# Performance work log

Measured on AMD Instinct MI355X. Metric: run time of the kernel, lower is better.

The kernel has to match this reference:

```python
import jax, jax.numpy as jnp
import numpy as np

D_MODEL = 2048
N_HEADS = 16
HEAD_DIM = D_MODEL // N_HEADS
SCALE = HEAD_DIM ** -0.5


def setup_inputs() -> dict:
    key = jax.random.key(0)
    ks = jax.random.split(key, 9)
    B, L, D = 4, 4096, D_MODEL
    s = 1.0 / np.sqrt(D)
    inp = {"x": jax.random.normal(ks[0], (B, L, D), dtype=jnp.float32)}
    inp["Wq"] = jax.random.normal(ks[1], (D, D), dtype=jnp.float32) * s
    inp["bq"] = jnp.zeros((D,), dtype=jnp.float32)
    inp["Wk"] = jax.random.normal(ks[2], (D, D), dtype=jnp.float32) * s
    inp["bk"] = jnp.zeros((D,), dtype=jnp.float32)
    inp["Wv"] = jax.random.normal(ks[3], (D, D), dtype=jnp.float32) * s
    inp["bv"] = jnp.zeros((D,), dtype=jnp.float32)
    inp["Wo"] = jax.random.normal(ks[4], (D, D), dtype=jnp.float32) * s
    inp["bo"] = jnp.zeros((D,), dtype=jnp.float32)
    return inp


def reference(x, Wq, bq, Wk, bk, Wv, bv, Wo, bo):
    B, L, D = x.shape
    H, Hd = N_HEADS, HEAD_DIM
    # projections (torch Linear: x @ W.T + b)
    q = jnp.einsum('bld,ed->ble', x, Wq) + bq
    k = jnp.einsum('bld,ed->ble', x, Wk) + bk
    v = jnp.einsum('bld,ed->ble', x, Wv) + bv
    phi_q = jax.nn.elu(q) + 1.0
    phi_k = jax.nn.elu(k) + 1.0
    # (B, L, H, Hd)
    phi_q = phi_q.reshape(B, L, H, Hd)
    phi_k = phi_k.reshape(B, L, H, Hd)
    v = v.reshape(B, L, H, Hd)
    # elementwise prefix sum over sequence dim
    kv_sum = jnp.cumsum(phi_k * v, axis=1)  # (B, L, H, Hd)
    context = (phi_q * kv_sum).reshape(B, L, D) * SCALE
    return jnp.einsum('bld,ed->ble', context, Wo) + bo
```

## Files before the change

### kernel.cpp

```cpp
#include <hip/hip_runtime.h>
#include <hip/hip_bf16.h>
#include <cstdint>
#include <cstddef>

typedef __bf16 bf16x8 __attribute__((ext_vector_type(8)));
typedef __bf16 bf16x4 __attribute__((ext_vector_type(4)));
typedef float  f32x4  __attribute__((ext_vector_type(4)));

#define D_MODEL 2048
#define SEQ     4096
#define BATCH   4
#define M_TOK   (BATCH * SEQ)
#define ATTN_SCALE 0.08838834764831845f

#define BM 256
#define BN 256
#define BK 64
#define NT (D_MODEL / BK)
#define BUF_BYTES 65536
#define B_OFF     32768

#define NSEG   64
#define SEGLEN (SEQ / NSEG)

__device__ __forceinline__ void async_load16(const void* g, void* l) {
    __builtin_amdgcn_global_load_lds(
        (const __attribute__((address_space(1))) unsigned int*)g,
        (__attribute__((address_space(3))) unsigned int*)l,
        16, 0, 0);
}

__device__ __forceinline__ void wg_barrier() {
    __builtin_amdgcn_sched_barrier(0);
    __builtin_amdgcn_s_barrier();
    __builtin_amdgcn_sched_barrier(0);
}

#define VMCNT(n) asm volatile("s_waitcnt vmcnt(" #n ")" ::: "memory")

__global__ __launch_bounds__(256) void k_cast_bf16(const float* __restrict__ in,
                                                   __bf16* __restrict__ out,
                                                   int n8) {
    int i = blockIdx.x * 256 + threadIdx.x;
    if (i >= n8) return;
    const float4* in4 = (const float4*)in;
    float4 a = in4[2 * i];
    float4 b = in4[2 * i + 1];
    bf16x8 o;
    o[0] = (__bf16)a.x; o[1] = (__bf16)a.y; o[2] = (__bf16)a.z; o[3] = (__bf16)a.w;
    o[4] = (__bf16)b.x; o[5] = (__bf16)b.y; o[6] = (__bf16)b.z; o[7] = (__bf16)b.w;
    ((bf16x8*)out)[i] = o;
}

__global__ __launch_bounds__(256) void k_cast_w4(const float* __restrict__ w0,
                                                 const float* __restrict__ w1,
                                                 const float* __restrict__ w2,
                                                 const float* __restrict__ w3,
                                                 __bf16* __restrict__ out, int n8) {
    const float* srcs[4] = {w0, w1, w2, w3};
    const float* in = srcs[blockIdx.y];
    __bf16* o = out + (size_t)blockIdx.y * (size_t)n8 * 8;
    int i = blockIdx.x * 256 + threadIdx.x;
    if (i >= n8) return;
    const float4* in4 = (const float4*)in;
    float4 a = in4[2 * i];
    float4 b = in4[2 * i + 1];
    bf16x8 v;
    v[0] = (__bf16)a.x; v[1] = (__bf16)a.y; v[2] = (__bf16)a.z; v[3] = (__bf16)a.w;
    v[4] = (__bf16)b.x; v[5] = (__bf16)b.y; v[6] = (__bf16)b.z; v[7] = (__bf16)b.w;
    ((bf16x8*)o)[i] = v;
}

template <int PHI, typename OUT_T>
__device__ __forceinline__ void gemm256(const __bf16* __restrict__ A,
                                        const __bf16* __restrict__ Bm,
                                        const float* __restrict__ bias,
                                        OUT_T* __restrict__ C,
                                        int bx, int by) {
    extern __shared__ bf16x8 lds_dyn[];
    char* lds = (char*)lds_dyn;

    const int tid  = threadIdx.x;
    const int lane = tid & 63;
    const int wave = tid >> 6;
    const int wr = wave & 1;
    const int wc = wave >> 1;
    const long bm = (long)by * BM;
    const long bn = (long)bx * BN;
    const int  K = D_MODEL, N = D_MODEL;

    const int sp  = tid & 7;
    const int rA0 = tid >> 3;
    const int rA1 = 64 + rA0;
    const int rBe = ((tid >> 8) << 6) + ((tid >> 3) & 31);
    const int rBo = rBe + 32;
    const __bf16* gA0 = A  + (bm + rA0) * (long)K + ((sp ^ (rA0 & 7)) << 3);
    const __bf16* gA1 = A  + (bm + rA1) * (long)K + ((sp ^ (rA1 & 7)) << 3);
    const __bf16* gBe = Bm + (bn + rBe) * (long)K + ((sp ^ (rBe & 7)) << 3);
    const __bf16* gBo = Bm + (bn + rBo) * (long)K + ((sp ^ (rBo & 7)) << 3);
    const long l128K = 128L * K;
    const int lA0 = tid * 16;
    const int lA1 = 8192 + tid * 16;
    const int lBe = B_OFF + ((tid >> 8) << 13) + (((tid >> 3) & 31) << 7) + sp * 16;
    const int lBo = lBe + 4096;

    auto issue2 = [&](const __bf16* g, int ldsByte) {
        async_load16(g, lds + ldsByte);
        async_load16(g + l128K, lds + ldsByte + 16384);
    };

    issue2(gA0, lA0);              gA0 += BK;
    issue2(gBe, lBe);              gBe += BK;
    issue2(gBo, lBo);              gBo += BK;
    issue2(gA1, lA1);              gA1 += BK;
    issue2(gA0, lA0 + BUF_BYTES);  gA0 += BK;
    issue2(gBe, lBe + BUF_BYTES);  gBe += BK;
    VMCNT(8);
    wg_barrier();

    const int lm   = lane & 15;
    const int ksel = lane >> 4;
    const int m3   = lm & 7;
    const int clo  = ksel ^ (m3 & 3);
    const int cb0  = ((((m3 >> 2) << 2) | clo) << 4);
    const int cb1  = ((((1 ^ (m3 >> 2)) << 2) | clo) << 4);
    const int aBase = (wr * 128 + lm) * 128;
    const int bBase = B_OFF + (wc * 64 + lm) * 128;

    f32x4 acc[8][4] = {};

    int cur = 0;
#pragma unroll 1
    for (int t = 0; t < NT; ++t) {
#pragma unroll
        for (int p = 0; p < 4; ++p) {
            const int qm = p >> 1, qn = p & 1;
            bf16x8 af[4][2], bfr[2][2];
#pragma unroll
            for (int i = 0; i < 4; ++i) {
                const char* rp = lds + cur + aBase + (qm * 64 + i * 16) * 128;
                af[i][0] = *(const bf16x8*)(rp + cb0);
                af[i][1] = *(const bf16x8*)(rp + cb1);
            }
#pragma unroll
            for (int j = 0; j < 2; ++j) {
                const char* rp = lds + cur + bBase + (qn * 32 + j * 16) * 128;
                bfr[j][0] = *(const bf16x8*)(rp + cb0);
                bfr[j][1] = *(const bf16x8*)(rp + cb1);
            }
            if (p == 0 && t + 1 < NT) { issue2(gBo, lBo + (cur ^ BUF_BYTES)); gBo += BK; }
            if (p == 1 && t + 1 < NT) { issue2(gA1, lA1 + (cur ^ BUF_BYTES)); gA1 += BK; }
            if (p == 2 && t + 2 < NT) { issue2(gA0, lA0 + cur); gA0 += BK; }
            if (p == 3 && t + 2 < NT) { issue2(gBe, lBe + cur); gBe += BK; }
            wg_barrier();
            __builtin_amdgcn_s_setprio(1);
#pragma unroll
            for (int s = 0; s < 2; ++s)
#pragma unroll
                for (int i = 0; i < 4; ++i)
#pragma unroll
                    for (int j = 0; j < 2; ++j)
                        acc[qm * 4 + i][qn * 2 + j] = __builtin_amdgcn_mfma_f32_16x16x32_bf16(
                            af[i][s], bfr[j][s], acc[qm * 4 + i][qn * 2 + j], 0, 0, 0);
            __builtin_amdgcn_s_setprio(0);
            if (p == 0 || p == 1) { if (t < NT - 1) VMCNT(8); }
            if (p == 3) { if (t < NT - 2) VMCNT(8); else if (t == NT - 2) VMCNT(0); }
            wg_barrier();
        }
        cur ^= BUF_BYTES;
    }

    const int r0m = (lane >> 4) << 2;
#pragma unroll
    for (int i = 0; i < 8; ++i) {
        const long mg = bm + wr * 128 + i * 16 + r0m;
#pragma unroll
        for (int j = 0; j < 4; ++j) {
            const long ng = bn + wc * 64 + j * 16 + lm;
            const float bia = bias[ng];
#pragma unroll
            for (int r = 0; r < 4; ++r) {
                float v = acc[i][j][r] + bia;
                if (PHI) v = (v > 0.f) ? (v + 1.f) : __expf(v);
                C[(mg + r) * (long)N + ng] = (OUT_T)v;
            }
        }
    }
}

__global__ __launch_bounds__(512, 2) void k_gemm_qkv(
    const __bf16* __restrict__ xb,
    const __bf16* __restrict__ wq, const __bf16* __restrict__ wk, const __bf16* __restrict__ wv,
    const float* __restrict__ bq, const float* __restrict__ bk, const float* __restrict__ bv,
    __bf16* __restrict__ oq, __bf16* __restrict__ ok, __bf16* __restrict__ ov) {
    const int flat = blockIdx.y * 8 + blockIdx.x;
    const int swz  = (flat & 7) * 64 + (flat >> 3);
    const int bx = swz & 7, by = swz >> 3;
    const int z = blockIdx.z;
    const __bf16* W = (z == 0) ? wq : (z == 1) ? wk : wv;
    const float*  b = (z == 0) ? bq : (z == 1) ? bk : bv;
    __bf16*       o = (z == 0) ? oq : (z == 1) ? ok : ov;
    if (z < 2)
        gemm256<1, __bf16>(xb, W, b, o, bx, by);
    else
        gemm256<0, __bf16>(xb, W, b, o, bx, by);
}

__global__ __launch_bounds__(512, 2) void k_gemm_out(
    const __bf16* __restrict__ ctx, const __bf16* __restrict__ wo,
    const float* __restrict__ bo, float* __restrict__ out) {
    const int flat = blockIdx.y * 8 + blockIdx.x;
    const int swz  = (flat & 7) * 64 + (flat >> 3);
    gemm256<0, float>(ctx, wo, bo, out, swz & 7, swz >> 3);
}

__global__ __launch_bounds__(256) void k_scan_partial(
    const __bf16* __restrict__ phik, const __bf16* __restrict__ v,
    float* __restrict__ partial) {
    const int b  = blockIdx.z;
    const int s  = blockIdx.y;
    const int c0 = blockIdx.x * 1024 + threadIdx.x * 4;
    long base = ((long)b * SEQ + (long)s * SEGLEN) * D_MODEL + c0;
    const bf16x4* pk = (const bf16x4*)(phik + base);
    const bf16x4* pv = (const bf16x4*)(v + base);
    float s0 = 0, s1 = 0, s2 = 0, s3 = 0;
    for (int l = 0; l < SEGLEN; l++) {
        bf16x4 a = *pk, w = *pv;
        s0 += (float)a[0] * (float)w[0];
        s1 += (float)a[1] * (float)w[1];
        s2 += (float)a[2] * (float)w[2];
        s3 += (float)a[3] * (float)w[3];
        pk += D_MODEL / 4; pv += D_MODEL / 4;
    }
    *(float4*)(partial + ((long)(b * NSEG + s)) * D_MODEL + c0) = make_float4(s0, s1, s2, s3);
}

__global__ __launch_bounds__(256) void k_scan_apply(
    const __bf16* __restrict__ phiq,
    __bf16* phik_ctx,
    const __bf16* __restrict__ v,
    const float* __restrict__ partial) {
    const int b  = blockIdx.z;
    const int s  = blockIdx.y;
    const int c0 = blockIdx.x * 1024 + threadIdx.x * 4;
    float r0 = 0, r1 = 0, r2 = 0, r3 = 0;
    for (int sp = 0; sp < s; sp++) {
        float4 p = *(const float4*)(partial + ((long)(b * NSEG + sp)) * D_MODEL + c0);
        r0 += p.x; r1 += p.y; r2 += p.z; r3 += p.w;
    }
    long base = ((long)b * SEQ + (long)s * SEGLEN) * D_MODEL + c0;
    bf16x4* pk = (bf16x4*)(phik_ctx + base);
    const bf16x4* pv = (const bf16x4*)(v + base);
    const bf16x4* pq = (const bf16x4*)(phiq + base);
    for (int l = 0; l < SEGLEN; l++) {
        bf16x4 a = *pk, w = *pv, q = *pq;
        r0 += (float)a[0] * (float)w[0];
        r1 += (float)a[1] * (float)w[1];
        r2 += (float)a[2] * (float)w[2];
        r3 += (float)a[3] * (float)w[3];
        bf16x4 o;
        o[0] = (__bf16)((float)q[0] * r0 * ATTN_SCALE);
        o[1] = (__bf16)((float)q[1] * r1 * ATTN_SCALE);
        o[2] = (__bf16)((float)q[2] * r2 * ATTN_SCALE);
        o[3] = (__bf16)((float)q[3] * r3 * ATTN_SCALE);
        *pk = o;
        pk += D_MODEL / 4; pv += D_MODEL / 4; pq += D_MODEL / 4;
    }
}

extern "C" void kernel_launch(void* const* d_in, const int* in_sizes, int n_in,
                              void* d_out, int out_size, void* d_ws, size_t ws_size,
                              hipStream_t stream) {
    const float* x  = (const float*)d_in[0];
    const float* Wq = (const float*)d_in[1];
    const float* bq = (const float*)d_in[2];
    const float* Wk = (const float*)d_in[3];
    const float* bk = (const float*)d_in[4];
    const float* Wv = (const float*)d_in[5];
    const float* bv = (const float*)d_in[6];
    const float* Wo = (const float*)d_in[7];
    const float* bo = (const float*)d_in[8];

    const size_t XB = (size_t)M_TOK * D_MODEL;
    const size_t WB = (size_t)D_MODEL * D_MODEL;

    char* p = (char*)d_ws;
    __bf16* xb   = (__bf16*)p; p += XB * 2;
    __bf16* wqb  = (__bf16*)p; p += WB * 2;
    __bf16* wkb  = (__bf16*)p; p += WB * 2;
    __bf16* wvb  = (__bf16*)p; p += WB * 2;
    __bf16* wob  = (__bf16*)p; p += WB * 2;
    __bf16* phiq = (__bf16*)p; p += XB * 2;
    __bf16* phik = (__bf16*)p; p += XB * 2;
    __bf16* vb   = (__bf16*)p; p += XB * 2;
    if ((size_t)(p - (char*)d_ws) > ws_size) return;

    float*  partial = (float*)xb;
    __bf16* ctx     = phik;

    static bool attr_done = false;
    if (!attr_done) {
        hipFuncSetAttribute(reinterpret_cast<const void*>(&k_gemm_qkv),
                            hipFuncAttributeMaxDynamicSharedMemorySize, 131072);
        hipFuncSetAttribute(reinterpret_cast<const void*>(&k_gemm_out),
                            hipFuncAttributeMaxDynamicSharedMemorySize, 131072);
        attr_done = true;
    }

    k_cast_bf16<<<dim3((unsigned)(XB / 8 / 256)), 256, 0, stream>>>(x, xb, (int)(XB / 8));
    k_cast_w4<<<dim3((unsigned)(WB / 8 / 256), 4), 256, 0, stream>>>(Wq, Wk, Wv, Wo, wqb, (int)(WB / 8));

    k_gemm_qkv<<<dim3(D_MODEL / BN, M_TOK / BM, 3), 512, 131072, stream>>>(
        xb, wqb, wkb, wvb, bq, bk, bv, phiq, phik, vb);

    k_scan_partial<<<dim3(2, NSEG, BATCH), 256, 0, stream>>>(phik, vb, partial);
    k_scan_apply<<<dim3(2, NSEG, BATCH), 256, 0, stream>>>(phiq, phik, vb, partial);

    k_gemm_out<<<dim3(D_MODEL / BN, M_TOK / BM, 1), 512, 131072, stream>>>(
        ctx, wob, bo, (float*)d_out);
}
```

Before: 882.7 us.

## Simplify GEMM main loop to one-tile prefetch with single barrier per K-step

Replaces the four-phase per-K-tile schedule, which interleaved partial prefetches two tiles ahead with two barriers per phase, with a plain double-buffered loop. The loop issues all loads for the next tile at the top, then runs two k-halves of 8x4 MFMAs from the current buffer. It ends with a full vmcnt(0) wait and one barrier per iteration. This cuts barrier and waitcnt overhead and simplifies instruction scheduling, but prefetch depth drops from two tiles to one. The full wait at each iteration end may leave global-load latency exposed.

```diff
diff --git a/kernel.cpp b/kernel.cpp
--- a/kernel.cpp
+++ b/kernel.cpp
@@ -109,13 +109,12 @@
         async_load16(g + l128K, lds + ldsByte + 16384);
     };
 
-    issue2(gA0, lA0);              gA0 += BK;
-    issue2(gBe, lBe);              gBe += BK;
-    issue2(gBo, lBo);              gBo += BK;
-    issue2(gA1, lA1);              gA1 += BK;
-    issue2(gA0, lA0 + BUF_BYTES);  gA0 += BK;
-    issue2(gBe, lBe + BUF_BYTES);  gBe += BK;
-    VMCNT(8);
+    issue2(gA0, lA0); gA0 += BK;
+    issue2(gBe, lBe); gBe += BK;
+    issue2(gBo, lBo); gBo += BK;
+    issue2(gA1, lA1); gA1 += BK;
+    __builtin_amdgcn_sched_barrier(0);
+    VMCNT(0);
     wg_barrier();
 
     const int lm   = lane & 15;
@@ -132,41 +131,36 @@
     int cur = 0;
 #pragma unroll 1
     for (int t = 0; t < NT; ++t) {
-#pragma unroll
-        for (int p = 0; p < 4; ++p) {
-            const int qm = p >> 1, qn = p & 1;
-            bf16x8 af[4][2], bfr[2][2];
-#pragma unroll
-            for (int i = 0; i < 4; ++i) {
-                const char* rp = lds + cur + aBase + (qm * 64 + i * 16) * 128;
-                af[i][0] = *(const bf16x8*)(rp + cb0);
-                af[i][1] = *(const bf16x8*)(rp + cb1);
-            }
-#pragma unroll
-            for (int j = 0; j < 2; ++j) {
-                const char* rp = lds + cur + bBase + (qn * 32 + j * 16) * 128;
-                bfr[j][0] = *(const bf16x8*)(rp + cb0);
-                bfr[j][1] = *(const bf16x8*)(rp + cb1);
-            }
-            if (p == 0 && t + 1 < NT) { issue2(gBo, lBo + (cur ^ BUF_BYTES)); gBo += BK; }
-            if (p == 1 && t + 1 < NT) { issue2(gA1, lA1 + (cur ^ BUF_BYTES)); gA1 += BK; }
-            if (p == 2 && t + 2 < NT) { issue2(gA0, lA0 + cur); gA0 += BK; }
-            if (p == 3 && t + 2 < NT) { issue2(gBe, lBe + cur); gBe += BK; }
-            wg_barrier();
+        const char* bufc = lds + cur;
+        const int stg = cur ^ BUF_BYTES;
+        if (t + 1 < NT) {
+            issue2(gA0, lA0 + stg); gA0 += BK;
+            issue2(gBe, lBe + stg); gBe += BK;
+            issue2(gBo, lBo + stg); gBo += BK;
+            issue2(gA1, lA1 + stg); gA1 += BK;
+        }
+#pragma unroll
+        for (int s = 0; s < 2; ++s) {
+            const int cbs = s ? cb1 : cb0;
+            bf16x8 af[8], bf[4];
+#pragma unroll
+            for (int i = 0; i < 8; ++i)
+                af[i] = *(const bf16x8*)(bufc + aBase + i * 2048 + cbs);
+#pragma unroll
+            for (int j = 0; j < 4; ++j)
+                bf[j] = *(const bf16x8*)(bufc + bBase + j * 2048 + cbs);
             __builtin_amdgcn_s_setprio(1);
 #pragma unroll
-            for (int s = 0; s < 2; ++s)
-#pragma unroll
-                for (int i = 0; i < 4; ++i)
-#pragma unroll
-                    for (int j = 0; j < 2; ++j)
-                        acc[qm * 4 + i][qn * 2 + j] = __builtin_amdgcn_mfma_f32_16x16x32_bf16(
-                            af[i][s], bfr[j][s], acc[qm * 4 + i][qn * 2 + j], 0, 0, 0);
+            for (int i = 0; i < 8; ++i)
+#pragma unroll
+                for (int j = 0; j < 4; ++j)
+                    acc[i][j] = __builtin_amdgcn_mfma_f32_16x16x32_bf16(
+                        af[i], bf[j], acc[i][j], 0, 0, 0);
             __builtin_amdgcn_s_setprio(0);
-            if (p == 0 || p == 1) { if (t < NT - 1) VMCNT(8); }
-            if (p == 3) { if (t < NT - 2) VMCNT(8); else if (t == NT - 2) VMCNT(0); }
-            wg_barrier();
         }
+        __builtin_amdgcn_sched_barrier(0);
+        if (t + 1 < NT) VMCNT(0);
+        wg_barrier();
         cur ^= BUF_BYTES;
     }
 
```

After: 799.8 us. 9.4% less time.
